# Optimization experiments

Hardware: AMD Instinct MI355X
Metric: run time of the kernel (lower is better)

Reference implementation:

```python
import jax, jax.numpy as jnp
import numpy as np

TOP_K = 2

def setup_inputs() -> dict:
    key = jax.random.key(0)
    ks = jax.random.split(key, 5)
    B, S, D, E, R, H = 4, 2048, 1024, 8, 128, 4096
    s = 0.02
    return {
        "hidden_states": jax.random.normal(ks[0], (B, S, D), jnp.float32),
        "w_route": jax.random.normal(ks[1], (E, D, R), jnp.float32) * s,
        "w3": jax.random.normal(ks[2], (E, D, H), jnp.float32) * s,
        "wr2h": jax.random.normal(ks[3], (E, R, H), jnp.float32) * s,
        "wh2d": jax.random.normal(ks[4], (E, H, D), jnp.float32) * s,
    }

def reference(hidden_states, w_route, w3, wr2h, wh2d):
    B, S, D = hidden_states.shape
    E = w_route.shape[0]
    x = hidden_states.reshape(-1, D)                      # [N, D]
    N = x.shape[0]
    # per-expert routing activations (also reused as w1_state inside experts)
    acts = jnp.einsum('nd,edr->ner', x, w_route)          # [N, E, R]
    norms = jnp.linalg.norm(acts, axis=-1)                # [N, E] router logits
    probs = jax.nn.softmax(norms.astype(jnp.float32), axis=-1)
    topw, sel = jax.lax.top_k(probs, TOP_K)               # [N, k]
    topw = topw / topw.sum(axis=-1, keepdims=True)
    topw = topw.astype(x.dtype)
    # dense combine weights: routing weight if expert selected, else 0
    combine = jnp.zeros((N, E), x.dtype).at[jnp.arange(N)[:, None], sel].add(topw)
    out = jnp.zeros_like(x)
    for e in range(E):  # fixed small expert count
        h = (x @ w3[e]) * jax.nn.silu(acts[:, e, :] @ wr2h[e])  # [N, H]
        out = out + (h @ wh2d[e]) * combine[:, e:e + 1]
    final = out.reshape(B, S, D)
    # load balancing loss on the router logits (expert_act_norms)
    mask = jax.nn.one_hot(sel, E, dtype=jnp.float32)      # [N, k, E]
    tokens_per_expert = mask.mean(axis=0)                 # [k, E]
    router_prob_per_expert = probs.mean(axis=0)           # [E]
    bl_loss = jnp.sum(tokens_per_expert * router_prob_per_expert[None, :]) * E
    return final, norms, bl_loss
```

## Files before the change

### kernel.cpp

```cpp
#include <hip/hip_runtime.h>


#define DEV static __device__ __forceinline__

typedef float  f32x4  __attribute__((ext_vector_type(4)));
typedef __bf16 bf16x8 __attribute__((ext_vector_type(8)));

#define VMCNT0() asm volatile("s_waitcnt vmcnt(0)" ::: "memory")
#define SBAR()   __builtin_amdgcn_s_barrier()

DEV unsigned short f2bf(float f) {
  union { float f; unsigned u; } v; v.f = f;
  unsigned r = v.u + 0x7fffu + ((v.u >> 16) & 1u);
  return (unsigned short)(r >> 16);
}
DEV float bf2f(unsigned short b) {
  union { unsigned u; float f; } v; v.u = ((unsigned)b) << 16;
  return v.f;
}

DEV void gll16(const void* g, void* l) {
  __builtin_amdgcn_global_load_lds(
      (const __attribute__((address_space(1))) unsigned int*)g,
      (__attribute__((address_space(3))) unsigned int*)l, 16, 0, 0);
}

DEV f32x4 mfma16(bf16x8 a, bf16x8 b, f32x4 c) {
  return __builtin_amdgcn_mfma_f32_16x16x32_bf16(a, b, c, 0, 0, 0);
}

DEV int xcd_swz_gen(int bid, int nwg) {
  int x = bid & 7, o = bid >> 3;
  int q = nwg >> 3, r = nwg & 7;
  return (x < r ? x * (q + 1) : r * (q + 1) + (x - r) * q) + o;
}

DEV int swz_slot(int s) {
  int p = s >> 3, w0 = (s & 7) ^ (p & 7);
  return (((p << 1) | (w0 >> 2)) << 2) | (w0 & 3);
}
DEV bf16x8 frag_read32(const unsigned short* lds, int row, int lg) {
  int p = row >> 1;
  int off = p * 128 + (((((row & 1) << 2) | lg) ^ (p & 7)) << 4);
  return *(const bf16x8*)((const char*)lds + off);
}

DEV bf16x8 frag_read(const unsigned short* lds, int row, int kb) {
  int off = row * 128 + ((kb * 2) ^ ((row & 7) << 4));
  return *(const bf16x8*)((const char*)lds + off);
}
DEV void stage_linear(const unsigned short* base, size_t pitch, int k0,
                      unsigned short* lds, int tid) {
  int wq = tid >> 6, lane = tid & 63;
#pragma unroll
  for (int i = 0; i < 4; ++i) {
    int s = wq * 256 + i * 64 + lane;
    int row = s >> 3, b = s & 7;
    int bb = b ^ (row & 7);
    const unsigned short* g = base + (size_t)row * pitch + (size_t)(k0 + bb * 8);
    gll16(g, lds + (size_t)(wq * 256 + i * 64) * 8);
  }
}


__global__ __launch_bounds__(256) void k_cast_x(const float* __restrict__ x,
    unsigned short* __restrict__ xh, unsigned short* __restrict__ xl) {
  int stride = gridDim.x * blockDim.x;
  for (int i = blockIdx.x * blockDim.x + threadIdx.x; i < 8192 * 1024 / 4;
       i += stride) {
    float4 v = ((const float4*)x)[i];
    ushort4 h, l;
    h.x = f2bf(v.x); l.x = f2bf(v.x - bf2f(h.x));
    h.y = f2bf(v.y); l.y = f2bf(v.y - bf2f(h.y));
    h.z = f2bf(v.z); l.z = f2bf(v.z - bf2f(h.z));
    h.w = f2bf(v.w); l.w = f2bf(v.w - bf2f(h.w));
    ((ushort4*)xh)[i] = h;
    ((ushort4*)xl)[i] = l;
  }
}

__global__ void k_zero(int* cnt, float* probsum) {
  int t = threadIdx.x;
  if (t < 16) cnt[t] = 0;
  if (t < 8)  probsum[t] = 0.f;
}

__global__ __launch_bounds__(256) void k_transp(const float* __restrict__ src,
    unsigned short* __restrict__ dst, int K, int N) {
  int ntn = N >> 6;
  int kt = blockIdx.x / ntn, nt = blockIdx.x % ntn;
  int e = blockIdx.y;
  __shared__ float tl[64][65];
  const float* s = src + (size_t)e * K * N;
  unsigned short* d = dst + (size_t)e * N * K;
  int tid = threadIdx.x;
  int c4 = (tid & 15) * 4, rr = tid >> 4;
#pragma unroll
  for (int p = 0; p < 4; ++p) {
    int row = rr + p * 16;
    float4 v = *(const float4*)(s + (size_t)(kt * 64 + row) * N + nt * 64 + c4);
    tl[row][c4] = v.x; tl[row][c4 + 1] = v.y;
    tl[row][c4 + 2] = v.z; tl[row][c4 + 3] = v.w;
  }
  __syncthreads();
#pragma unroll
  for (int p = 0; p < 4; ++p) {
    int n = rr + p * 16;
    ushort4 o;
    o.x = f2bf(tl[c4 + 0][n]); o.y = f2bf(tl[c4 + 1][n]);
    o.z = f2bf(tl[c4 + 2][n]); o.w = f2bf(tl[c4 + 3][n]);
    *(ushort4*)(d + (size_t)(nt * 64 + n) * K + kt * 64 + c4) = o;
  }
}

__global__ __launch_bounds__(256) void k_transp_split(const float* __restrict__ src,
    unsigned short* __restrict__ dh, unsigned short* __restrict__ dl, int K, int N) {
  int ntn = N >> 6;
  int kt = blockIdx.x / ntn, nt = blockIdx.x % ntn;
  int e = blockIdx.y;
  __shared__ float tl[64][65];
  const float* s = src + (size_t)e * K * N;
  size_t dbase = (size_t)e * N * K;
  int tid = threadIdx.x;
  int c4 = (tid & 15) * 4, rr = tid >> 4;
#pragma unroll
  for (int p = 0; p < 4; ++p) {
    int row = rr + p * 16;
    float4 v = *(const float4*)(s + (size_t)(kt * 64 + row) * N + nt * 64 + c4);
    tl[row][c4] = v.x; tl[row][c4 + 1] = v.y;
    tl[row][c4 + 2] = v.z; tl[row][c4 + 3] = v.w;
  }
  __syncthreads();
#pragma unroll
  for (int p = 0; p < 4; ++p) {
    int n = rr + p * 16;
    ushort4 oh, ol;
#pragma unroll
    for (int i = 0; i < 4; ++i) {
      float v = tl[c4 + i][n];
      unsigned short hh = f2bf(v);
      unsigned short ll = f2bf(v - bf2f(hh));
      ((unsigned short*)&oh)[i] = hh;
      ((unsigned short*)&ol)[i] = ll;
    }
    *(ushort4*)(dh + dbase + (size_t)(nt * 64 + n) * K + kt * 64 + c4) = oh;
    *(ushort4*)(dl + dbase + (size_t)(nt * 64 + n) * K + kt * 64 + c4) = ol;
  }
}

__global__ __launch_bounds__(256) void k_route_gemm(
    const unsigned short* __restrict__ xh, const unsigned short* __restrict__ xl,
    const unsigned short* __restrict__ wrh_t, const unsigned short* __restrict__ wrl_t,
    unsigned short* __restrict__ acts, float* __restrict__ norms_out) {
  __shared__ __align__(16) unsigned short Ah[128 * 64], Al[128 * 64];
  __shared__ __align__(16) unsigned short Bh[128 * 64], Bl[128 * 64];
  __shared__ float ssq_s[128][2];
  int tid = threadIdx.x;
  int mt = blockIdx.x, e = blockIdx.y;
  int wq = tid >> 6, lane = tid & 63;
  int wm = wq >> 1, wn = wq & 1, lg = lane >> 4, lc = lane & 15;
  f32x4 acc[4][4] = {};
  const unsigned short* ah_src = xh + (size_t)mt * 128 * 1024;
  const unsigned short* al_src = xl + (size_t)mt * 128 * 1024;
  const unsigned short* bh_src = wrh_t + (size_t)e * 128 * 1024;
  const unsigned short* bl_src = wrl_t + (size_t)e * 128 * 1024;
  for (int kt = 0; kt < 16; ++kt) {
    int k0 = kt * 64;
    stage_linear(ah_src, 1024, k0, Ah, tid);
    stage_linear(al_src, 1024, k0, Al, tid);
    stage_linear(bh_src, 1024, k0, Bh, tid);
    stage_linear(bl_src, 1024, k0, Bl, tid);
    __syncthreads();
#pragma unroll
    for (int ks = 0; ks < 2; ++ks) {
      int kb = ks * 32 + lg * 8;
      bf16x8 ahf[4], alf[4], bhf[4], blf[4];
#pragma unroll
      for (int i = 0; i < 4; ++i) {
        ahf[i] = frag_read(Ah, wm * 64 + i * 16 + lc, kb);
        alf[i] = frag_read(Al, wm * 64 + i * 16 + lc, kb);
        bhf[i] = frag_read(Bh, wn * 64 + i * 16 + lc, kb);
        blf[i] = frag_read(Bl, wn * 64 + i * 16 + lc, kb);
      }
#pragma unroll
      for (int mf = 0; mf < 4; ++mf)
#pragma unroll
        for (int nf = 0; nf < 4; ++nf) {
          acc[mf][nf] = mfma16(ahf[mf], bhf[nf], acc[mf][nf]);
          acc[mf][nf] = mfma16(alf[mf], bhf[nf], acc[mf][nf]);
          acc[mf][nf] = mfma16(ahf[mf], blf[nf], acc[mf][nf]);
        }
    }
    __syncthreads();
  }
  float ssq[4][4];
#pragma unroll
  for (int mf = 0; mf < 4; ++mf)
#pragma unroll
    for (int r = 0; r < 4; ++r) ssq[mf][r] = 0.f;
#pragma unroll
  for (int mf = 0; mf < 4; ++mf)
#pragma unroll
    for (int nf = 0; nf < 4; ++nf)
#pragma unroll
      for (int r = 0; r < 4; ++r) {
        float v = acc[mf][nf][r];
        int row = wm * 64 + mf * 16 + lg * 4 + r;
        int col = wn * 64 + nf * 16 + lc;
        acts[(size_t)(mt * 128 + row) * 1024 + e * 128 + col] = f2bf(v);
        ssq[mf][r] += v * v;
      }
#pragma unroll
  for (int mf = 0; mf < 4; ++mf)
#pragma unroll
    for (int r = 0; r < 4; ++r) {
      float s = ssq[mf][r];
      s += __shfl_xor(s, 1); s += __shfl_xor(s, 2);
      s += __shfl_xor(s, 4); s += __shfl_xor(s, 8);
      if (lc == 0) ssq_s[wm * 64 + mf * 16 + lg * 4 + r][wn] = s;
    }
  __syncthreads();
  if (tid < 128) {
    float s = ssq_s[tid][0] + ssq_s[tid][1];
    norms_out[(size_t)(mt * 128 + tid) * 8 + e] = sqrtf(s);
  }
}

__global__ __launch_bounds__(256) void k_router(const float* __restrict__ norms,
    float* __restrict__ topw, int* __restrict__ sel,
    int* __restrict__ cnt, float* __restrict__ probsum) {
  __shared__ float ps_s[8];
  __shared__ int cnt_s[16];
  int tid = threadIdx.x;
  if (tid < 8)  ps_s[tid] = 0.f;
  if (tid < 16) cnt_s[tid] = 0;
  __syncthreads();
  int n = blockIdx.x * 256 + tid;
  float p[8], mx = -3.4e38f;
#pragma unroll
  for (int e = 0; e < 8; ++e) { p[e] = norms[(size_t)n * 8 + e]; mx = fmaxf(mx, p[e]); }
  float s = 0.f;
#pragma unroll
  for (int e = 0; e < 8; ++e) { p[e] = __expf(p[e] - mx); s += p[e]; }
  float inv = 1.f / s;
  int i1 = 0; float v1 = p[0];
#pragma unroll
  for (int e = 1; e < 8; ++e) if (p[e] > v1) { v1 = p[e]; i1 = e; }
  int i2 = -1; float v2 = -1.f;
#pragma unroll
  for (int e = 0; e < 8; ++e) if (e != i1 && p[e] > v2) { v2 = p[e]; i2 = e; }
  float wsum = v1 + v2;
  topw[n * 2 + 0] = v1 / wsum;
  topw[n * 2 + 1] = v2 / wsum;
  sel[n * 2 + 0] = i1;
  sel[n * 2 + 1] = i2;
  atomicAdd(&cnt_s[i1], 1);
  atomicAdd(&cnt_s[8 + i2], 1);
#pragma unroll
  for (int e = 0; e < 8; ++e) atomicAdd(&ps_s[e], p[e] * inv);
  __syncthreads();
  if (tid < 8)  atomicAdd(&probsum[tid], ps_s[tid]);
  if (tid < 16) atomicAdd(&cnt[tid], cnt_s[tid]);
}

__global__ void k_plan(const int* __restrict__ cnt, const float* __restrict__ probsum,
                       int* __restrict__ offs, int* __restrict__ fill,
                       int4* __restrict__ tilemap, float* __restrict__ bl_out) {
  int4* map256 = tilemap;
  int4* map128 = tilemap + 80;
  int t = 0;
  for (int k = 0; k < 2; ++k) {
    int pos = 0;
    for (int e = 0; e < 8; ++e) {
      int c = cnt[k * 8 + e];
      offs[k * 8 + e] = pos;
      int ntl = (c + 255) >> 8;
      for (int i = 0; i < ntl; ++i) {
        int rr = c - i * 256; if (rr > 256) rr = 256;
        map256[t] = make_int4(e, k * 8192 + pos + i * 256, rr, 0);
        ++t;
      }
      pos += c;
    }
  }
  for (; t < 80; ++t) map256[t] = make_int4(0, 0, 0, 0);
  for (int i = 0; i < 80; ++i) {
    int4 m = map256[i];
    for (int h = 0; h < 2; ++h) {
      int r = m.z - h * 128;
      if (r < 0) r = 0; if (r > 128) r = 128;
      map128[i * 2 + h] = make_int4(m.x, m.y + h * 128, r, i * 256 + h * 128);
    }
  }
  for (int i = 0; i < 16; ++i) fill[i] = 0;
  float bl = 0.f;
  for (int e = 0; e < 8; ++e)
    bl += ((float)(cnt[e] + cnt[8 + e]) / 8192.f) * (probsum[e] / 8192.f);
  *bl_out = bl * 8.f;
}

__global__ __launch_bounds__(256) void k_fill(const int* __restrict__ sel,
    const float* __restrict__ topw, const int* __restrict__ offs,
    int* __restrict__ fill, int* __restrict__ list01, float* __restrict__ wlist) {
  int n = blockIdx.x * 256 + threadIdx.x;
#pragma unroll
  for (int k = 0; k < 2; ++k) {
    int e = sel[n * 2 + k];
    int pos = atomicAdd(&fill[k * 8 + e], 1);
    int idx = k * 8192 + offs[k * 8 + e] + pos;
    list01[idx] = n;
    wlist[idx] = topw[n * 2 + k];
  }
}

__global__ __launch_bounds__(512, 2) void k_gemm1(
    const unsigned short* __restrict__ xh, const unsigned short* __restrict__ acts,
    const unsigned short* __restrict__ w3t, const unsigned short* __restrict__ wr2h_t,
    const int* __restrict__ list, const int4* __restrict__ tilemap, int tile_lo,
    int nt, unsigned short* __restrict__ hbuf) {
  __shared__ __align__(16) unsigned short SA[2][256 * 32];
  __shared__ __align__(16) unsigned short SB[2][128 * 32];
  __shared__ int toks[256];
  int wg = xcd_swz_gen((int)blockIdx.x, nt * 32);
  int tloc = wg >> 5, bn = wg & 31;
  int4 ent = tilemap[tile_lo + tloc];
  int e = ent.x, posbase = ent.y, rows = ent.z;
  if (rows == 0) return;
  int tid = threadIdx.x;
  if (tid < 256) {
    int rr = tid < rows ? tid : rows - 1;
    toks[tid] = list[posbase + rr];
  }
  __syncthreads();
  int wq = tid >> 6, lane = tid & 63;
  int wm = wq >> 1, wn = wq & 1, lg = lane >> 4, lc = lane & 15;
  int sA0 = tid, sA1 = tid + 512;
  int sB0 = tid;
  int vA0 = swz_slot(sA0), vA1 = swz_slot(sA1), vB0 = swz_slot(sB0);
  const unsigned short* gA0 = xh + (size_t)toks[vA0 >> 2] * 1024 + (vA0 & 3) * 8;
  const unsigned short* gA1 = xh + (size_t)toks[vA1 >> 2] * 1024 + (vA1 & 3) * 8;
  const unsigned short* qA0 = acts + (size_t)toks[vA0 >> 2] * 1024 + e * 128 + (vA0 & 3) * 8;
  const unsigned short* qA1 = acts + (size_t)toks[vA1 >> 2] * 1024 + e * 128 + (vA1 & 3) * 8;
  const unsigned short* gB0 =
      w3t + ((size_t)e * 4096 + bn * 128 + (vB0 >> 2)) * 1024 + (vB0 & 3) * 8;
  const unsigned short* qB0 =
      wr2h_t + ((size_t)e * 4096 + bn * 128 + (vB0 >> 2)) * 128 + (vB0 & 3) * 8;
  f32x4 acc_a[4][4] = {}, acc_s[4][4] = {};

  auto stage1 = [&](int tt, int bs) {
    unsigned short* dA0 = &SA[bs][(size_t)sA0 * 8];
    unsigned short* dA1 = &SA[bs][(size_t)sA1 * 8];
    unsigned short* dB0 = &SB[bs][(size_t)sB0 * 8];
    if (tt < 32) {
      int k0 = tt * 32;
      gll16(gA0 + k0, dA0); gll16(gA1 + k0, dA1); gll16(gB0 + k0, dB0);
    } else {
      int k0 = (tt - 32) * 32;
      gll16(qA0 + k0, dA0); gll16(qA1 + k0, dA1); gll16(qB0 + k0, dB0);
    }
  };

  stage1(0, 0);
  VMCNT0();
  SBAR();
  int cur = 0;

#define G1_STEP(T, ACC, DOSTAGE)                                             \
  {                                                                          \
    if (DOSTAGE) stage1((T) + 1, cur ^ 1);                                   \
    bf16x8 af[4], bv[4];                                                     \
    _Pragma("unroll") for (int i = 0; i < 4; ++i)                            \
      af[i] = frag_read32(&SA[cur][0], wm * 64 + i * 16 + lc, lg);           \
    _Pragma("unroll") for (int i = 0; i < 4; ++i)                            \
      bv[i] = frag_read32(&SB[cur][0], wn * 64 + i * 16 + lc, lg);           \
    __builtin_amdgcn_s_setprio(1);                                           \
    _Pragma("unroll") for (int mf = 0; mf < 4; ++mf)                         \
      _Pragma("unroll") for (int nf = 0; nf < 4; ++nf)                       \
        ACC[mf][nf] = mfma16(af[mf], bv[nf], ACC[mf][nf]);                   \
    __builtin_amdgcn_s_setprio(0);                                           \
    VMCNT0();                                                                \
    SBAR();                                                                  \
    cur ^= 1;                                                                \
  }

  for (int t = 0; t < 32; ++t) G1_STEP(t, acc_a, true);
  for (int t = 32; t < 36; ++t) G1_STEP(t, acc_s, t < 35);
#undef G1_STEP

  size_t hrow0 = (size_t)tloc * 256;
#pragma unroll
  for (int mf = 0; mf < 4; ++mf)
#pragma unroll
    for (int nf = 0; nf < 4; ++nf)
#pragma unroll
      for (int r = 0; r < 4; ++r) {
        int row = wm * 64 + mf * 16 + lg * 4 + r;
        if (row < rows) {
          int col = wn * 64 + nf * 16 + lc;
          float sv = acc_s[mf][nf][r];
          float hv = acc_a[mf][nf][r] * (sv / (1.f + __expf(-sv)));
          hbuf[(hrow0 + row) * 4096 + (size_t)bn * 128 + col] = f2bf(hv);
        }
      }
}

__global__ __launch_bounds__(512, 4) void k_gemm2(
    const unsigned short* __restrict__ hbuf, const unsigned short* __restrict__ wh2dt,
    const int* __restrict__ list, const float* __restrict__ wlist,
    const int4* __restrict__ map128, int tile_lo, int nt,
    float* __restrict__ out) {
  __shared__ __align__(16) unsigned short SA[2][128 * 32];
  __shared__ __align__(16) unsigned short SB[2][256 * 32];
  __shared__ int toks[128];
  __shared__ float wr_s[128];
  int wg = xcd_swz_gen((int)blockIdx.x, nt * 8);
  int tloc = wg >> 2, bn = wg & 3;
  int4 ent = map128[tile_lo * 2 + tloc];
  int e = ent.x, posbase = ent.y, rows = ent.z;
  if (rows == 0) return;
  int hb = ent.w - tile_lo * 256;
  int tid = threadIdx.x;
  if (tid < 128) {
    int rr = tid < rows ? tid : rows - 1;
    toks[tid] = list[posbase + rr];
    wr_s[tid] = wlist[posbase + rr];
  }
  __syncthreads();
  int wq = tid >> 6, lane = tid & 63;
  int wm = wq >> 2, wn = wq & 3, lg = lane >> 4, lc = lane & 15;
  int sA0 = tid;
  int sB0 = tid, sB1 = tid + 512;
  int vA0 = swz_slot(sA0), vB0 = swz_slot(sB0), vB1 = swz_slot(sB1);
  const unsigned short* gA0 = hbuf + (size_t)(hb + (vA0 >> 2)) * 4096 + (vA0 & 3) * 8;
  const unsigned short* gB0 =
      wh2dt + ((size_t)e * 1024 + bn * 256 + (vB0 >> 2)) * 4096 + (vB0 & 3) * 8;
  const unsigned short* gB1 =
      wh2dt + ((size_t)e * 1024 + bn * 256 + (vB1 >> 2)) * 4096 + (vB1 & 3) * 8;
  f32x4 acc[4][4] = {};

  auto stage2 = [&](int tt, int bs) {
    int k0 = tt * 32;
    gll16(gA0 + k0, &SA[bs][(size_t)sA0 * 8]);
    gll16(gB0 + k0, &SB[bs][(size_t)sB0 * 8]);
    gll16(gB1 + k0, &SB[bs][(size_t)sB1 * 8]);
  };

  stage2(0, 0);
  VMCNT0();
  SBAR();
  int cur = 0;

  for (int t = 0; t < 128; ++t) {
    if (t < 127) stage2(t + 1, cur ^ 1);
    bf16x8 af[4], bv[4];
#pragma unroll
    for (int i = 0; i < 4; ++i)
      af[i] = frag_read32(&SA[cur][0], wm * 64 + i * 16 + lc, lg);
#pragma unroll
    for (int i = 0; i < 4; ++i)
      bv[i] = frag_read32(&SB[cur][0], wn * 64 + i * 16 + lc, lg);
    __builtin_amdgcn_s_setprio(1);
#pragma unroll
    for (int mf = 0; mf < 4; ++mf)
#pragma unroll
      for (int nf = 0; nf < 4; ++nf)
        acc[mf][nf] = mfma16(af[mf], bv[nf], acc[mf][nf]);
    __builtin_amdgcn_s_setprio(0);
    VMCNT0();
    SBAR();
    cur ^= 1;
  }

#pragma unroll
  for (int mf = 0; mf < 4; ++mf)
#pragma unroll
    for (int nf = 0; nf < 4; ++nf)
#pragma unroll
      for (int r = 0; r < 4; ++r) {
        int row = wm * 64 + mf * 16 + lg * 4 + r;
        if (row < rows) {
          int col = wn * 64 + nf * 16 + lc;
          float v = acc[mf][nf][r] * wr_s[row];
          atomicAdd(out + (size_t)toks[row] * 1024 + bn * 256 + col, v);
        }
      }
}


extern "C" void kernel_launch(void* const* d_in, const int* in_sizes, int n_in,
                              void* d_out, int out_size, void* d_ws, size_t ws_size,
                              hipStream_t stream) {
  (void)in_sizes; (void)n_in; (void)out_size;
  const float* x      = (const float*)d_in[0];
  const float* wroute = (const float*)d_in[1];
  const float* w3     = (const float*)d_in[2];
  const float* wr2h   = (const float*)d_in[3];
  const float* wh2d   = (const float*)d_in[4];
  float* out = (float*)d_out;

  char* ws = (char*)d_ws;
  size_t off = 0;
  auto carve = [&](size_t bytes) -> void* {
    void* p = ws + off; off += (bytes + 255) & ~(size_t)255; return p;
  };
  unsigned short* xh     = (unsigned short*)carve((size_t)8192 * 1024 * 2);
  unsigned short* xl     = (unsigned short*)carve((size_t)8192 * 1024 * 2);
  unsigned short* wrh_t  = (unsigned short*)carve((size_t)8 * 128 * 1024 * 2);
  unsigned short* wrl_t  = (unsigned short*)carve((size_t)8 * 128 * 1024 * 2);
  unsigned short* w3t    = (unsigned short*)carve((size_t)8 * 4096 * 1024 * 2);
  unsigned short* wr2h_t = (unsigned short*)carve((size_t)8 * 4096 * 128 * 2);
  unsigned short* wh2dt  = (unsigned short*)carve((size_t)8 * 1024 * 4096 * 2);
  unsigned short* acts   = (unsigned short*)carve((size_t)8192 * 1024 * 2);
  int*   list01 = (int*)carve(2 * 8192 * 4);
  float* wlist  = (float*)carve(2 * 8192 * 4);
  int*   sel    = (int*)carve(8192 * 2 * 4);
  float* topw   = (float*)carve(8192 * 2 * 4);
  int*   ctr    = (int*)carve(8192);
  int* cnt = ctr; int* fill = ctr + 16; int* offs = ctr + 32;
  float* probsum = (float*)(ctr + 48);
  int4* tilemap = (int4*)(ctr + 64);

  size_t avail = ws_size > off ? ws_size - off : 0;
  int tpc = 0;
  const int cands[4] = {80, 40, 20, 10};
  for (int i = 0; i < 4; ++i) {
    if ((size_t)cands[i] * 256 * 4096 * 2 <= avail) { tpc = cands[i]; break; }
  }
  if (!tpc) return;
  unsigned short* hbuf = (unsigned short*)(ws + off);

  float* norms_out = out + 8388608;
  float* bl_out    = out + 8454144;

  hipMemsetAsync(out, 0, (size_t)8388608 * 4, stream);
  k_cast_x<<<2048, 256, 0, stream>>>(x, xh, xl);
  k_zero<<<1, 64, 0, stream>>>(cnt, probsum);
  k_transp<<<dim3(16 * 64, 8), 256, 0, stream>>>(w3, w3t, 1024, 4096);
  k_transp<<<dim3(64 * 16, 8), 256, 0, stream>>>(wh2d, wh2dt, 4096, 1024);
  k_transp<<<dim3(2 * 64, 8), 256, 0, stream>>>(wr2h, wr2h_t, 128, 4096);
  k_transp_split<<<dim3(16 * 2, 8), 256, 0, stream>>>(wroute, wrh_t, wrl_t, 1024, 128);
  k_route_gemm<<<dim3(64, 8), 256, 0, stream>>>(xh, xl, wrh_t, wrl_t, acts, norms_out);
  k_router<<<32, 256, 0, stream>>>(norms_out, topw, sel, cnt, probsum);
  k_plan<<<1, 1, 0, stream>>>(cnt, probsum, offs, fill, tilemap, bl_out);
  k_fill<<<32, 256, 0, stream>>>(sel, topw, offs, fill, list01, wlist);

  int nchunk = (80 + tpc - 1) / tpc;
  for (int c = 0; c < nchunk; ++c) {
    int tile_lo = c * tpc;
    int nt = 80 - tile_lo < tpc ? 80 - tile_lo : tpc;
    k_gemm1<<<nt * 32, 512, 0, stream>>>(
        xh, acts, w3t, wr2h_t, list01, tilemap, tile_lo, nt, hbuf);
    k_gemm2<<<nt * 8, 512, 0, stream>>>(
        hbuf, wh2dt, list01, wlist, tilemap + 80, tile_lo, nt, out);
  }
}
```

Before: 902.2 us.

## Triple-buffer LDS staging in both MoE GEMMs with partial vmcnt waits

Both grouped GEMM kernels move from a double-buffered LDS pipeline, which drained all global loads each step, to a three-stage ring that keeps two tiles in flight. Each step waits with vmcnt(3), so only the oldest tile's loads must have landed, and one barrier per step protects the buffer being refilled. The aim is to hide global-to-LDS latency behind MFMA work. The cost is 50% more LDS, and k_gemm2's launch bound drops from 4 to 2 blocks per CU, which can reduce occupancy.

Result: slower. 979.9 us (+8.6%).

```diff
diff --git a/kernel.cpp b/kernel.cpp
--- a/kernel.cpp
+++ b/kernel.cpp
@@ -6,7 +6,8 @@
 typedef float  f32x4  __attribute__((ext_vector_type(4)));
 typedef __bf16 bf16x8 __attribute__((ext_vector_type(8)));
 
-#define VMCNT0() asm volatile("s_waitcnt vmcnt(0)" ::: "memory")
+#define VMCNT_(n) asm volatile("s_waitcnt vmcnt(" #n ")" ::: "memory")
+#define VMCNT(n) VMCNT_(n)
 #define SBAR()   __builtin_amdgcn_s_barrier()
 
 DEV unsigned short f2bf(float f) {
@@ -318,8 +319,8 @@
     const unsigned short* __restrict__ w3t, const unsigned short* __restrict__ wr2h_t,
     const int* __restrict__ list, const int4* __restrict__ tilemap, int tile_lo,
     int nt, unsigned short* __restrict__ hbuf) {
-  __shared__ __align__(16) unsigned short SA[2][256 * 32];
-  __shared__ __align__(16) unsigned short SB[2][128 * 32];
+  __shared__ __align__(16) unsigned short SA[3][256 * 32];
+  __shared__ __align__(16) unsigned short SB[3][128 * 32];
   __shared__ int toks[256];
   int wg = xcd_swz_gen((int)blockIdx.x, nt * 32);
   int tloc = wg >> 5, bn = wg & 31;
@@ -359,33 +360,39 @@
       gll16(qA0 + k0, dA0); gll16(qA1 + k0, dA1); gll16(qB0 + k0, dB0);
     }
   };
-
-  stage1(0, 0);
-  VMCNT0();
-  SBAR();
-  int cur = 0;
-
-#define G1_STEP(T, ACC, DOSTAGE)                                             \
-  {                                                                          \
-    if (DOSTAGE) stage1((T) + 1, cur ^ 1);                                   \
-    bf16x8 af[4], bv[4];                                                     \
-    _Pragma("unroll") for (int i = 0; i < 4; ++i)                            \
-      af[i] = frag_read32(&SA[cur][0], wm * 64 + i * 16 + lc, lg);           \
-    _Pragma("unroll") for (int i = 0; i < 4; ++i)                            \
-      bv[i] = frag_read32(&SB[cur][0], wn * 64 + i * 16 + lc, lg);           \
-    __builtin_amdgcn_s_setprio(1);                                           \
-    _Pragma("unroll") for (int mf = 0; mf < 4; ++mf)                         \
-      _Pragma("unroll") for (int nf = 0; nf < 4; ++nf)                       \
-        ACC[mf][nf] = mfma16(af[mf], bv[nf], ACC[mf][nf]);                   \
-    __builtin_amdgcn_s_setprio(0);                                           \
-    VMCNT0();                                                                \
-    SBAR();                                                                  \
-    cur ^= 1;                                                                \
-  }
-
-  for (int t = 0; t < 32; ++t) G1_STEP(t, acc_a, true);
-  for (int t = 32; t < 36; ++t) G1_STEP(t, acc_s, t < 35);
-#undef G1_STEP
+  auto body1 = [&](int bufi, f32x4 (&ACC)[4][4]) {
+    bf16x8 af[4], bv[4];
+#pragma unroll
+    for (int i = 0; i < 4; ++i)
+      af[i] = frag_read32(&SA[bufi][0], wm * 64 + i * 16 + lc, lg);
+#pragma unroll
+    for (int i = 0; i < 4; ++i)
+      bv[i] = frag_read32(&SB[bufi][0], wn * 64 + i * 16 + lc, lg);
+    __builtin_amdgcn_s_setprio(1);
+#pragma unroll
+    for (int mf = 0; mf < 4; ++mf)
+#pragma unroll
+      for (int nf = 0; nf < 4; ++nf)
+        ACC[mf][nf] = mfma16(af[mf], bv[nf], ACC[mf][nf]);
+    __builtin_amdgcn_s_setprio(0);
+  };
+
+  stage1(0, 0); stage1(1, 1);
+  int cur = 0, bs = 2;
+  for (int t = 0; t < 32; ++t) {
+    VMCNT(3); SBAR();
+    stage1(t + 2, bs);
+    body1(cur, acc_a);
+    cur = cur == 2 ? 0 : cur + 1;
+    bs  = bs  == 2 ? 0 : bs  + 1;
+  }
+  VMCNT(3); SBAR(); stage1(34, bs); body1(cur, acc_s);
+  cur = cur == 2 ? 0 : cur + 1; bs = bs == 2 ? 0 : bs + 1;
+  VMCNT(3); SBAR(); stage1(35, bs); body1(cur, acc_s);
+  cur = cur == 2 ? 0 : cur + 1;
+  VMCNT(3); SBAR(); body1(cur, acc_s);
+  cur = cur == 2 ? 0 : cur + 1;
+  VMCNT(0); SBAR(); body1(cur, acc_s);
 
   size_t hrow0 = (size_t)tloc * 256;
 #pragma unroll
@@ -404,13 +411,13 @@
       }
 }
 
-__global__ __launch_bounds__(512, 4) void k_gemm2(
+__global__ __launch_bounds__(512, 2) void k_gemm2(
     const unsigned short* __restrict__ hbuf, const unsigned short* __restrict__ wh2dt,
     const int* __restrict__ list, const float* __restrict__ wlist,
     const int4* __restrict__ map128, int tile_lo, int nt,
     float* __restrict__ out) {
-  __shared__ __align__(16) unsigned short SA[2][128 * 32];
-  __shared__ __align__(16) unsigned short SB[2][256 * 32];
+  __shared__ __align__(16) unsigned short SA[3][128 * 32];
+  __shared__ __align__(16) unsigned short SB[3][256 * 32];
   __shared__ int toks[128];
   __shared__ float wr_s[128];
   int wg = xcd_swz_gen((int)blockIdx.x, nt * 8);
@@ -444,21 +451,14 @@
     gll16(gB0 + k0, &SB[bs][(size_t)sB0 * 8]);
     gll16(gB1 + k0, &SB[bs][(size_t)sB1 * 8]);
   };
-
-  stage2(0, 0);
-  VMCNT0();
-  SBAR();
-  int cur = 0;
-
-  for (int t = 0; t < 128; ++t) {
-    if (t < 127) stage2(t + 1, cur ^ 1);
+  auto body2 = [&](int bufi) {
     bf16x8 af[4], bv[4];
 #pragma unroll
     for (int i = 0; i < 4; ++i)
-      af[i] = frag_read32(&SA[cur][0], wm * 64 + i * 16 + lc, lg);
+      af[i] = frag_read32(&SA[bufi][0], wm * 64 + i * 16 + lc, lg);
 #pragma unroll
     for (int i = 0; i < 4; ++i)
-      bv[i] = frag_read32(&SB[cur][0], wn * 64 + i * 16 + lc, lg);
+      bv[i] = frag_read32(&SB[bufi][0], wn * 64 + i * 16 + lc, lg);
     __builtin_amdgcn_s_setprio(1);
 #pragma unroll
     for (int mf = 0; mf < 4; ++mf)
@@ -466,10 +466,20 @@
       for (int nf = 0; nf < 4; ++nf)
         acc[mf][nf] = mfma16(af[mf], bv[nf], acc[mf][nf]);
     __builtin_amdgcn_s_setprio(0);
-    VMCNT0();
-    SBAR();
-    cur ^= 1;
-  }
+  };
+
+  stage2(0, 0); stage2(1, 1);
+  int cur = 0, bs = 2;
+  for (int t = 0; t < 126; ++t) {
+    VMCNT(3); SBAR();
+    stage2(t + 2, bs);
+    body2(cur);
+    cur = cur == 2 ? 0 : cur + 1;
+    bs  = bs  == 2 ? 0 : bs  + 1;
+  }
+  VMCNT(3); SBAR(); body2(cur);
+  cur = cur == 2 ? 0 : cur + 1;
+  VMCNT(0); SBAR(); body2(cur);
 
 #pragma unroll
   for (int mf = 0; mf < 4; ++mf)
```
